# Performance work log

Hardware: AMD Instinct MI355X
Metric: run time of the kernel (lower is better)

## Reference

```python
import jax, jax.numpy as jnp
import numpy as np

DIM = 512
NUM_HEADS = 16
D_HEAD = DIM // NUM_HEADS
B, S = 4, 1024


def _relative_shift(pos_score):
    # pos_score: [B, H, S1, S2] -> Transformer-XL relative shift
    b, h, s1, s2 = pos_score.shape
    padded = jnp.pad(pos_score, ((0, 0), (0, 0), (0, 0), (1, 0)))  # [B,H,S1,S2+1]
    padded = padded.reshape(b, h, s2 + 1, s1)
    return padded[:, :, 1:].reshape(b, h, s1, s2)


def setup_inputs() -> dict:
    key = jax.random.key(0)
    ks = jax.random.split(key, 16)
    f32 = jnp.float32
    scale = 0.02
    inp = {
        "query": jax.random.normal(ks[0], (B, S, DIM), f32),
        "key": jax.random.normal(ks[1], (B, S, DIM), f32),
        "value": jax.random.normal(ks[2], (B, S, DIM), f32),
        "pos_embedding": jax.random.normal(ks[3], (B, S, DIM), f32),
        "Wq": jax.random.normal(ks[4], (DIM, DIM), f32) * scale,
        "bq": jnp.zeros((DIM,), f32),
        "Wk": jax.random.normal(ks[5], (DIM, DIM), f32) * scale,
        "bk": jnp.zeros((DIM,), f32),
        "Wv": jax.random.normal(ks[6], (DIM, DIM), f32) * scale,
        "bv": jnp.zeros((DIM,), f32),
        "Wp": jax.random.normal(ks[7], (DIM, DIM), f32) * scale,  # pos_proj, no bias
        "u_bias": jax.random.normal(ks[8], (NUM_HEADS, D_HEAD), f32) * scale,
        "v_bias": jax.random.normal(ks[9], (NUM_HEADS, D_HEAD), f32) * scale,
        "Wo": jax.random.normal(ks[10], (DIM, DIM), f32) * scale,
        "bo": jnp.zeros((DIM,), f32),
    }
    return inp


def reference(query, key, value, pos_embedding, Wq, bq, Wk, bk, Wv, bv, Wp,
              u_bias, v_bias, Wo, bo):
    b = query.shape[0]
    # projections (torch Linear: x @ W.T + b), split heads -> [B, S, H, Dh]
    q = (query @ Wq.T + bq).reshape(b, -1, NUM_HEADS, D_HEAD)
    k = (key @ Wk.T + bk).reshape(b, -1, NUM_HEADS, D_HEAD)
    v = (value @ Wv.T + bv).reshape(b, -1, NUM_HEADS, D_HEAD)
    p = (pos_embedding @ Wp.T).reshape(b, -1, NUM_HEADS, D_HEAD)

    # content score: (q + u) @ k^T  -> [B, H, Sq, Sk]
    content_score = jnp.einsum('bqhd,bkhd->bhqk', q + u_bias, k)
    # position score: (q + v) @ pos^T, then relative shift
    pos_score = jnp.einsum('bqhd,bkhd->bhqk', q + v_bias, p)
    pos_score = _relative_shift(pos_score)

    score = (content_score + pos_score) / np.sqrt(D_HEAD).astype(np.float32)
    attn = jax.nn.softmax(score, axis=-1)  # dropout_p = 0.0 -> identity

    context = jnp.einsum('bhqk,bkhd->bqhd', attn, v).reshape(b, -1, DIM)
    return context @ Wo.T + bo
```

## Files before the change

kernel.cpp:

```cpp
#include <hip/hip_runtime.h>
#include <hip/hip_bf16.h>
#include <math.h>


typedef float f32x4 __attribute__((ext_vector_type(4)));
typedef __bf16 bf16x8 __attribute__((ext_vector_type(8)));
typedef __bf16 bf16x2 __attribute__((ext_vector_type(2)));

#define MFMA16(a, b, c) __builtin_amdgcn_mfma_f32_16x16x32_bf16((a), (b), (c), 0, 0, 0)

constexpr int Bb  = 4;
constexpr int S   = 1024;
constexpr int H   = 16;
constexpr int Dh  = 32;
constexpr int DIM = 512;
constexpr float SCALEL2E = 0.25501818637084186f;
constexpr int ZROWS = 3 * S + 16;
constexpr size_t ZN = (size_t)64 * ZROWS * Dh;

constexpr size_t XN = (size_t)Bb * S * DIM;
constexpr size_t WN = (size_t)DIM * DIM;

__device__ inline bf16x8 cvt8(const float* __restrict__ p) {
  f32x4 a = *(const f32x4*)p;
  f32x4 b = *(const f32x4*)(p + 4);
  bf16x8 r;
  r[0] = (__bf16)a[0]; r[1] = (__bf16)a[1]; r[2] = (__bf16)a[2]; r[3] = (__bf16)a[3];
  r[4] = (__bf16)b[0]; r[5] = (__bf16)b[1]; r[6] = (__bf16)b[2]; r[7] = (__bf16)b[3];
  return r;
}

__device__ inline float fexp2(float x) {
  float r;
  asm("v_exp_f32 %0, %1" : "=v"(r) : "v"(x));
  return r;
}

__device__ inline void gload_lds16(const __bf16* g, __bf16* l) {
  __builtin_amdgcn_global_load_lds(
      (const __attribute__((address_space(1))) unsigned int*)g,
      (__attribute__((address_space(3))) unsigned int*)l, 16, 0, 0);
}

__global__ __launch_bounds__(256) void conv_kernel(
    const float* __restrict__ q, const float* __restrict__ k,
    const float* __restrict__ v, const float* __restrict__ p,
    const float* __restrict__ wq, const float* __restrict__ wk,
    const float* __restrict__ wv, const float* __restrict__ wp,
    const float* __restrict__ wo,
    __bf16* __restrict__ xb, __bf16* __restrict__ wb,
    __bf16* __restrict__ phZ)
{
  const int y = blockIdx.y;
  if (y >= 9) {
    const size_t i = (((size_t)(y - 9) * 1024 + blockIdx.x) * 256 + threadIdx.x) * 8;
    if (i < ZN) {
      bf16x8 zz = {};
      *(bf16x8*)(phZ + i) = zz;
    }
    return;
  }
  const float* src;
  size_t n;
  __bf16* dst;
  if (y < 4) {
    src = (y == 0) ? q : (y == 1) ? k : (y == 2) ? v : p;
    n = XN;
    dst = xb + (size_t)y * XN;
  } else {
    const int w = y - 4;
    src = (w == 0) ? wq : (w == 1) ? wk : (w == 2) ? wv : (w == 3) ? wp : wo;
    n = WN;
    dst = wb + (size_t)w * WN;
  }
  const size_t i = ((size_t)blockIdx.x * 256 + threadIdx.x) * 8;
  if (i >= n) return;
  *(bf16x8*)(dst + i) = cvt8(src + i);
}

__global__ __launch_bounds__(256) void gemm_kernel(
    const __bf16* __restrict__ xb, const __bf16* __restrict__ wb,
    const __bf16* __restrict__ ctxp,
    const float* __restrict__ bq, const float* __restrict__ bk,
    const float* __restrict__ bv, const float* __restrict__ bo,
    const float* __restrict__ ub, const float* __restrict__ vb,
    __bf16* __restrict__ qu, __bf16* __restrict__ qv,
    __bf16* __restrict__ kk, __bf16* __restrict__ vt,
    __bf16* __restrict__ phZ,
    float* __restrict__ outp, int mode)
{
  __shared__ __align__(16) __bf16 As[128 * 64];
  __shared__ __align__(16) __bf16 Bs[128 * 64];

  const int bid = blockIdx.x;
  const int u = bid >> 3;
  const int by = u & 3;
  const int idx = (bid & 7) + 8 * (u >> 2);
  int bx, z;
  if (mode == 0) { bx = idx & 31; z = idx >> 5; }
  else           { bx = idx;      z = 4; }

  const __bf16* Ag = (z < 4) ? (xb + (size_t)z * XN) : ctxp;
  const __bf16* Bg = wb + (size_t)z * WN;

  const int tid = threadIdx.x;
  const int wid = tid >> 6;
  const int ln = tid & 63;
  const int lm = ln & 15, lg = ln >> 4;
  const int wr = wid >> 1, wc = wid & 1;
  const int brow = bx * 128;
  const int bcol = by * 128;

  const int srow = ln >> 3;
  const int sc   = ln & 7;

  f32x4 acc[4][4] = {};

  for (int kt = 0; kt < DIM / 64; ++kt) {
    const int k0 = kt * 64;
#pragma unroll
    for (int i = 0; i < 4; ++i) {
      const int rb = wid * 32 + i * 8;
      const int r = rb + srow;
      const int cg = sc ^ (r & 7);
      gload_lds16(Ag + (size_t)(brow + r) * DIM + k0 + cg * 8, &As[rb * 64]);
      gload_lds16(Bg + (size_t)(bcol + r) * DIM + k0 + cg * 8, &Bs[rb * 64]);
    }
    __syncthreads();

#pragma unroll
    for (int ks = 0; ks < 2; ++ks) {
      bf16x8 a[4], b[4];
#pragma unroll
      for (int m = 0; m < 4; ++m) {
        const int row = wr * 64 + m * 16 + lm;
        const int cc = (ks * 4 + lg) ^ (row & 7);
        a[m] = *(const bf16x8*)&As[row * 64 + cc * 8];
      }
#pragma unroll
      for (int n = 0; n < 4; ++n) {
        const int row = wc * 64 + n * 16 + lm;
        const int cc = (ks * 4 + lg) ^ (row & 7);
        b[n] = *(const bf16x8*)&Bs[row * 64 + cc * 8];
      }
#pragma unroll
      for (int m = 0; m < 4; ++m)
#pragma unroll
        for (int n = 0; n < 4; ++n)
          acc[m][n] = MFMA16(a[m], b[n], acc[m][n]);
    }
    __syncthreads();
  }

#pragma unroll
  for (int n = 0; n < 4; ++n) {
    const int o = bcol + wc * 64 + n * 16 + lm;
    float bias = 0.f, ubv = 0.f, vbv = 0.f;
    if (z == 0) { bias = bq[o]; ubv = ub[o]; vbv = vb[o]; }
    else if (z == 1) bias = bk[o];
    else if (z == 2) bias = bv[o];
    else if (z == 4) bias = bo[o];
    const int h = o >> 5, d = o & 31;
#pragma unroll
    for (int m = 0; m < 4; ++m) {
#pragma unroll
      for (int r = 0; r < 4; ++r) {
        const int M = brow + wr * 64 + m * 16 + lg * 4 + r;
        const float val = acc[m][n][r];
        if (z == 4) {
          outp[(size_t)M * DIM + o] = val + bias;
          continue;
        }
        const int b = M >> 10, s = M & (S - 1);
        const int bh = b * H + h;
        if (z == 0) {
          const size_t idx2 = ((size_t)bh * S + s) * Dh + d;
          qu[idx2] = (__bf16)((val + bias + ubv) * SCALEL2E);
          qv[idx2] = (__bf16)((val + bias + vbv) * SCALEL2E);
        } else if (z == 1) {
          kk[((size_t)bh * S + s) * Dh + d] = (__bf16)(val + bias);
        } else if (z == 2) {
          const int t = s & 31;
          const int sp = (s & ~31) | ((t < 16) ? (t << 1) : ((t << 1) - 31));
          vt[((size_t)bh * Dh + d) * S + sp] = (__bf16)(val + bias);
        } else {
          phZ[((size_t)bh * ZROWS + (S + 1 + s)) * Dh + d] = (__bf16)val;
        }
      }
    }
  }
}

__global__ __launch_bounds__(256, 4) void attn_kernel(
    const __bf16* __restrict__ qu, const __bf16* __restrict__ qv,
    const __bf16* __restrict__ kk, const __bf16* __restrict__ vt,
    const __bf16* __restrict__ phZ,
    __bf16* __restrict__ ctx)
{
  __shared__ __align__(16) __bf16 kv_lds[4][2][1024];
  __shared__ __align__(16) __bf16 at_all[4][2][16 * 40];

  const int tid = threadIdx.x;
  const int wid = tid >> 6;
  const int l = tid & 63;
  const int lm = l & 15, lg = l >> 4;

  const int bid = blockIdx.x;
  const int bh = (bid & 7) + 8 * ((bid >> 3) & 7);
  const int q0 = (bid >> 6) * 64 + wid * 16;
  const int h = bh & (H - 1), b = bh >> 4;

  const __bf16* qub = qu + (size_t)bh * S * Dh;
  const __bf16* qvb = qv + (size_t)bh * S * Dh;
  const __bf16* kb  = kk + (size_t)bh * S * Dh;
  const __bf16* vtb = vt + (size_t)bh * Dh * S;
  const __bf16* pZb = phZ + (size_t)bh * ZROWS * Dh;
  const __bf16* pAb = pZb + (size_t)(S + 1) * Dh;

  const bf16x8 au  = *(const bf16x8*)(qub + (size_t)(q0 + lm) * Dh + lg * 8);
  const bf16x8 avA = *(const bf16x8*)(qvb + (size_t)(q0 + lm) * Dh + lg * 8);
  const bf16x8 avB = *(const bf16x8*)(qvb + (size_t)(q0 + 1 + lm) * Dh + lg * 8);

  int  slr[4];
  bool prd[4];
#pragma unroll
  for (int r = 0; r < 4; ++r) {
    const int qr = lg * 4 + r;
    slr[r] = (l & 48) | ((lm - qr + 15) & 15);
    prd[r] = (lm <= qr);
  }

  bf16x8 ones8;
#pragma unroll
  for (int i = 0; i < 8; ++i) ones8[i] = (__bf16)1.0f;

  f32x4 cta = {0.f,0.f,0.f,0.f}, ctb = {0.f,0.f,0.f,0.f};
  f32x4 ls  = {0.f,0.f,0.f,0.f};
  const f32x4 zero4 = {0.f,0.f,0.f,0.f};

  const int srow = l >> 2;
  const int scg  = ((l & 3) ^ (srow & 3)) * 8;
  auto stage = [&](int kt, int buf) {
    const __bf16* src;
    if (wid == 0)      src = kb  + (size_t)(kt + srow) * Dh + scg;
    else if (wid == 1) src = kb  + (size_t)(kt + 16 + srow) * Dh + scg;
    else if (wid == 2) src = vtb + (size_t)srow * S + kt + scg;
    else               src = vtb + (size_t)(16 + srow) * S + kt + scg;
    gload_lds16(src, &kv_lds[buf][wid >> 1][(wid & 1) * 512]);
  };

  const int cc = (lg ^ (lm & 3)) * 8;

  auto zwin = [&](int kt, bf16x8& z0, bf16x8& z1, bf16x8& z2, bool& uB) {
    const int ktc = (kt < S) ? kt : (S - 32);
    uB = (ktc > q0 - 31);
    const int mb = ktc - q0 + (S - 16);
    const __bf16* zb = uB ? pZb : pAb;
    z0 = *(const bf16x8*)(zb + (size_t)(mb + lm) * Dh + lg * 8);
    z1 = *(const bf16x8*)(zb + (size_t)(mb + 16 + lm) * Dh + lg * 8);
    z2 = *(const bf16x8*)(zb + (size_t)(mb + 32 + lm) * Dh + lg * 8);
  };

  auto half = [&](int kt, int tb, __bf16* at,
                  bf16x8 z0, bf16x8 z1, bf16x8 z2, bool uB) {
    const __bf16* Ks = kv_lds[tb][0];
    const __bf16* Vs = kv_lds[tb][1];
    bf16x8 kf0 = *(const bf16x8*)(Ks + lm * 32 + cc);
    bf16x8 kf1 = *(const bf16x8*)(Ks + (lm + 16) * 32 + cc);
    __builtin_amdgcn_s_setprio(1);
    f32x4 c0 = MFMA16(au, kf0, zero4);
    f32x4 c1 = MFMA16(au, kf1, zero4);
    const bf16x8 av = uB ? avB : avA;
    f32x4 pt0 = MFMA16(av, z0, zero4);
    f32x4 pt1 = MFMA16(av, z1, zero4);
    f32x4 pt2 = MFMA16(av, z2, zero4);
    __builtin_amdgcn_s_setprio(0);
    if (uB && (kt < q0 + 16)) {
      const int mb = kt - q0 + (S - 16);
      bf16x8 y0 = *(const bf16x8*)(pAb + (size_t)(mb + lm) * Dh + lg * 8);
      bf16x8 y1 = *(const bf16x8*)(pAb + (size_t)(mb + 16 + lm) * Dh + lg * 8);
      bf16x8 y2 = *(const bf16x8*)(pAb + (size_t)(mb + 32 + lm) * Dh + lg * 8);
      pt0 = MFMA16(avA, y0, pt0);
      pt1 = MFMA16(avA, y1, pt1);
      pt2 = MFMA16(avA, y2, pt2);
    }

#pragma unroll
    for (int r = 0; r < 4; ++r) {
      const float v0 = __shfl(pt0[r], slr[r], 64);
      const float v1 = __shfl(pt1[r], slr[r], 64);
      const float v2 = __shfl(pt2[r], slr[r], 64);
      const float s0 = c0[r] + (prd[r] ? v0 : v1);
      const float s1 = c1[r] + (prd[r] ? v1 : v2);
      bf16x2 pp;
      pp[0] = (__bf16)fexp2(s0);
      pp[1] = (__bf16)fexp2(s1);
      *(bf16x2*)(at + (lg * 4 + r) * 40 + 2 * lm) = pp;
    }

    bf16x8 af  = *(const bf16x8*)(at + lm * 40 + lg * 8);
    bf16x8 vf0 = *(const bf16x8*)(Vs + lm * 32 + cc);
    bf16x8 vf1 = *(const bf16x8*)(Vs + (lm + 16) * 32 + cc);
    __builtin_amdgcn_s_setprio(1);
    cta = MFMA16(af, vf0, cta);
    ctb = MFMA16(af, vf1, ctb);
    ls  = MFMA16(af, ones8, ls);
    __builtin_amdgcn_s_setprio(0);
  };

  __bf16* at0 = at_all[wid][0];
  __bf16* at1 = at_all[wid][1];

  bf16x8 zA0, zA1, zA2, zB0, zB1, zB2;
  bool uA, uB;
  zwin(0, zA0, zA1, zA2, uA);
  stage(0, 0);
  stage(32, 1);
  asm volatile("s_waitcnt vmcnt(0)" ::: "memory");
  __builtin_amdgcn_s_barrier();

  for (int kt = 0; kt < S; kt += 64) {
    const int t = kt >> 5;
    stage((kt + 64 < S) ? kt + 64 : kt, (t + 2) & 3);
    stage((kt + 96 < S) ? kt + 96 : kt, (t + 3) & 3);
    zwin(kt + 32, zB0, zB1, zB2, uB);
    half(kt, t & 3, at0, zA0, zA1, zA2, uA);
    zwin(kt + 64, zA0, zA1, zA2, uA);
    half(kt + 32, (t + 1) & 3, at1, zB0, zB1, zB2, uB);

    asm volatile("s_waitcnt vmcnt(3)" ::: "memory");
    __builtin_amdgcn_s_barrier();
  }

#pragma unroll
  for (int r = 0; r < 4; ++r) {
    const int s0 = q0 + lg * 4 + r;
    const float inv = 1.f / ls[r];
    __bf16* cp = ctx + ((size_t)b * S + s0) * DIM + h * Dh;
    cp[lm]      = (__bf16)(cta[r] * inv);
    cp[16 + lm] = (__bf16)(ctb[r] * inv);
  }
}

extern "C" void kernel_launch(void* const* d_in, const int* in_sizes, int n_in,
                              void* d_out, int out_size, void* d_ws, size_t ws_size,
                              hipStream_t stream) {
  const float* query = (const float*)d_in[0];
  const float* key   = (const float*)d_in[1];
  const float* value = (const float*)d_in[2];
  const float* pos   = (const float*)d_in[3];
  const float* Wq = (const float*)d_in[4];
  const float* bq = (const float*)d_in[5];
  const float* Wk = (const float*)d_in[6];
  const float* bk = (const float*)d_in[7];
  const float* Wv = (const float*)d_in[8];
  const float* bv = (const float*)d_in[9];
  const float* Wp = (const float*)d_in[10];
  const float* ub = (const float*)d_in[11];
  const float* vb = (const float*)d_in[12];
  const float* Wo = (const float*)d_in[13];
  const float* bo = (const float*)d_in[14];
  float* out = (float*)d_out;

  char* ws = (char*)d_ws;
  const size_t MB = 1ull << 20;
  __bf16* xb  = (__bf16*)(ws + 0 * MB);
  __bf16* wb  = (__bf16*)(ws + 16 * MB);
  __bf16* qu  = (__bf16*)(ws + 19 * MB);
  __bf16* qv  = (__bf16*)(ws + 23 * MB);
  __bf16* kk  = (__bf16*)(ws + 27 * MB);
  __bf16* vt  = (__bf16*)(ws + 31 * MB);
  __bf16* phZ = (__bf16*)(ws + 35 * MB);
  __bf16* ctx = (__bf16*)(ws + 48 * MB);

  conv_kernel<<<dim3(1024, 13), dim3(256), 0, stream>>>(
      query, key, value, pos, Wq, Wk, Wv, Wp, Wo, xb, wb, phZ);

  gemm_kernel<<<dim3(512), dim3(256), 0, stream>>>(
      xb, wb, ctx, bq, bk, bv, bo, ub, vb,
      qu, qv, kk, vt, phZ, out, 0);

  attn_kernel<<<dim3(1024), dim3(256), 0, stream>>>(
      qu, qv, kk, vt, phZ, ctx);

  gemm_kernel<<<dim3(128), dim3(256), 0, stream>>>(
      xb, wb, ctx, bq, bk, bv, bo, ub, vb,
      qu, qv, kk, vt, phZ, out, 1);
}
```

Measured before the change: 95.62 us.

## Trim phZ zeroing, coalesce V-transpose store, halve output GEMM tile, unpermute V

The zero-fill of the padded position buffer now writes only the boundary row windows the attention kernel reads, not the whole buffer. The V projection epilogue stages results through swizzled LDS so it can write the transposed V with 16-byte coalesced stores, and it drops the interleaved sequence permutation. The attention kernel now writes P in natural column order to match. The output GEMM is templated with a 64-row M tile and launches twice as many blocks to fill more CUs. The risk is that rows left uninitialized in phZ might be read, and that the layout change must agree exactly between the producer and consumer kernels.

```diff
diff --git a/kernel.cpp b/kernel.cpp
--- a/kernel.cpp
+++ b/kernel.cpp
@@ -5,7 +5,7 @@
 
 typedef float f32x4 __attribute__((ext_vector_type(4)));
 typedef __bf16 bf16x8 __attribute__((ext_vector_type(8)));
-typedef __bf16 bf16x2 __attribute__((ext_vector_type(2)));
+typedef __bf16 bf16x4 __attribute__((ext_vector_type(4)));
 
 #define MFMA16(a, b, c) __builtin_amdgcn_mfma_f32_16x16x32_bf16((a), (b), (c), 0, 0, 0)
 
@@ -16,7 +16,6 @@
 constexpr int DIM = 512;
 constexpr float SCALEL2E = 0.25501818637084186f;
 constexpr int ZROWS = 3 * S + 16;
-constexpr size_t ZN = (size_t)64 * ZROWS * Dh;
 
 constexpr size_t XN = (size_t)Bb * S * DIM;
 constexpr size_t WN = (size_t)DIM * DIM;
@@ -52,11 +51,15 @@
     __bf16* __restrict__ phZ)
 {
   const int y = blockIdx.y;
-  if (y >= 9) {
-    const size_t i = (((size_t)(y - 9) * 1024 + blockIdx.x) * 256 + threadIdx.x) * 8;
-    if (i < ZN) {
+  if (y == 9) {
+    const int e8 = blockIdx.x * 256 + threadIdx.x;
+    if (e8 < 64 * 136 * 4) {
+      const int rowIdx = e8 >> 2, chunk = e8 & 3;
+      const int bh = rowIdx / 136;
+      const int rl = rowIdx - bh * 136;
+      const int row = (rl < 72) ? (960 + rl) : (2040 + (rl - 72));
       bf16x8 zz = {};
-      *(bf16x8*)(phZ + i) = zz;
+      *(bf16x8*)(phZ + ((size_t)bh * ZROWS + row) * Dh + chunk * 8) = zz;
     }
     return;
   }
@@ -78,6 +81,7 @@
   *(bf16x8*)(dst + i) = cvt8(src + i);
 }
 
+template <int MODE>
 __global__ __launch_bounds__(256) void gemm_kernel(
     const __bf16* __restrict__ xb, const __bf16* __restrict__ wb,
     const __bf16* __restrict__ ctxp,
@@ -87,17 +91,21 @@
     __bf16* __restrict__ qu, __bf16* __restrict__ qv,
     __bf16* __restrict__ kk, __bf16* __restrict__ vt,
     __bf16* __restrict__ phZ,
-    float* __restrict__ outp, int mode)
+    float* __restrict__ outp)
 {
-  __shared__ __align__(16) __bf16 As[128 * 64];
-  __shared__ __align__(16) __bf16 Bs[128 * 64];
+  constexpr int MR = (MODE == 0) ? 4 : 2;
+  constexpr int BM = MR * 32;
+  __shared__ __align__(16) __bf16 smem[BM * 64 + 128 * 64];
+  __bf16* As = smem;
+  __bf16* Bs = smem + BM * 64;
+  __bf16* trans = smem;
 
   const int bid = blockIdx.x;
   const int u = bid >> 3;
   const int by = u & 3;
   const int idx = (bid & 7) + 8 * (u >> 2);
   int bx, z;
-  if (mode == 0) { bx = idx & 31; z = idx >> 5; }
+  if (MODE == 0) { bx = idx & 31; z = idx >> 5; }
   else           { bx = idx;      z = 4; }
 
   const __bf16* Ag = (z < 4) ? (xb + (size_t)z * XN) : ctxp;
@@ -108,32 +116,38 @@
   const int ln = tid & 63;
   const int lm = ln & 15, lg = ln >> 4;
   const int wr = wid >> 1, wc = wid & 1;
-  const int brow = bx * 128;
+  const int brow = bx * BM;
   const int bcol = by * 128;
 
   const int srow = ln >> 3;
   const int sc   = ln & 7;
 
-  f32x4 acc[4][4] = {};
+  f32x4 acc[MR][4] = {};
 
   for (int kt = 0; kt < DIM / 64; ++kt) {
     const int k0 = kt * 64;
+#pragma unroll
+    for (int i = 0; i < MR; ++i) {
+      const int rb = wid * (MR * 8) + i * 8;
+      const int r = rb + srow;
+      const int cg = sc ^ (r & 7);
+      gload_lds16(Ag + (size_t)(brow + r) * DIM + k0 + cg * 8, &As[rb * 64]);
+    }
 #pragma unroll
     for (int i = 0; i < 4; ++i) {
       const int rb = wid * 32 + i * 8;
       const int r = rb + srow;
       const int cg = sc ^ (r & 7);
-      gload_lds16(Ag + (size_t)(brow + r) * DIM + k0 + cg * 8, &As[rb * 64]);
       gload_lds16(Bg + (size_t)(bcol + r) * DIM + k0 + cg * 8, &Bs[rb * 64]);
     }
     __syncthreads();
 
 #pragma unroll
     for (int ks = 0; ks < 2; ++ks) {
-      bf16x8 a[4], b[4];
-#pragma unroll
-      for (int m = 0; m < 4; ++m) {
-        const int row = wr * 64 + m * 16 + lm;
+      bf16x8 a[MR], b[4];
+#pragma unroll
+      for (int m = 0; m < MR; ++m) {
+        const int row = wr * (MR * 16) + m * 16 + lm;
         const int cc = (ks * 4 + lg) ^ (row & 7);
         a[m] = *(const bf16x8*)&As[row * 64 + cc * 8];
       }
@@ -144,12 +158,45 @@
         b[n] = *(const bf16x8*)&Bs[row * 64 + cc * 8];
       }
 #pragma unroll
-      for (int m = 0; m < 4; ++m)
+      for (int m = 0; m < MR; ++m)
 #pragma unroll
         for (int n = 0; n < 4; ++n)
           acc[m][n] = MFMA16(a[m], b[n], acc[m][n]);
     }
     __syncthreads();
+  }
+
+  if (MODE == 0 && z == 2) {
+    const int b = brow >> 10;
+    const int sbase = brow & (S - 1);
+#pragma unroll
+    for (int n = 0; n < 4; ++n) {
+      const int dl = wc * 64 + n * 16 + lm;
+      const float bias = bv[bcol + dl];
+#pragma unroll
+      for (int m = 0; m < 4; ++m) {
+        const int sl = wr * 64 + m * 16 + lg * 4;
+        bf16x4 pk;
+#pragma unroll
+        for (int r = 0; r < 4; ++r) pk[r] = (__bf16)(acc[m][n][r] + bias);
+        const int base = dl * 128 + (((sl >> 3) ^ (dl & 15)) * 8) + (sl & 7);
+        *(bf16x4*)(trans + base) = pk;
+      }
+    }
+    __syncthreads();
+#pragma unroll
+    for (int j = 0; j < 4; ++j) {
+      const int dl = (tid >> 3) + j * 32;
+      const int d = dl & 31, hl = dl >> 5;
+      const int cp = (tid & 7) * 2;
+      bf16x8 v0 = *(const bf16x8*)(trans + dl * 128 + ((cp ^ (dl & 15)) * 8));
+      bf16x8 v1 = *(const bf16x8*)(trans + dl * 128 + (((cp + 1) ^ (dl & 15)) * 8));
+      const int bh2 = b * H + (bcol >> 5) + hl;
+      __bf16* dst = vt + ((size_t)bh2 * Dh + d) * S + sbase + cp * 8;
+      *(bf16x8*)dst = v0;
+      *(bf16x8*)(dst + 8) = v1;
+    }
+    return;
   }
 
 #pragma unroll
@@ -158,14 +205,13 @@
     float bias = 0.f, ubv = 0.f, vbv = 0.f;
     if (z == 0) { bias = bq[o]; ubv = ub[o]; vbv = vb[o]; }
     else if (z == 1) bias = bk[o];
-    else if (z == 2) bias = bv[o];
     else if (z == 4) bias = bo[o];
     const int h = o >> 5, d = o & 31;
 #pragma unroll
-    for (int m = 0; m < 4; ++m) {
+    for (int m = 0; m < MR; ++m) {
 #pragma unroll
       for (int r = 0; r < 4; ++r) {
-        const int M = brow + wr * 64 + m * 16 + lg * 4 + r;
+        const int M = brow + wr * (MR * 16) + m * 16 + lg * 4 + r;
         const float val = acc[m][n][r];
         if (z == 4) {
           outp[(size_t)M * DIM + o] = val + bias;
@@ -179,10 +225,6 @@
           qv[idx2] = (__bf16)((val + bias + vbv) * SCALEL2E);
         } else if (z == 1) {
           kk[((size_t)bh * S + s) * Dh + d] = (__bf16)(val + bias);
-        } else if (z == 2) {
-          const int t = s & 31;
-          const int sp = (s & ~31) | ((t < 16) ? (t << 1) : ((t << 1) - 31));
-          vt[((size_t)bh * Dh + d) * S + sp] = (__bf16)(val + bias);
         } else {
           phZ[((size_t)bh * ZROWS + (S + 1 + s)) * Dh + d] = (__bf16)val;
         }
@@ -292,10 +334,8 @@
       const float v2 = __shfl(pt2[r], slr[r], 64);
       const float s0 = c0[r] + (prd[r] ? v0 : v1);
       const float s1 = c1[r] + (prd[r] ? v1 : v2);
-      bf16x2 pp;
-      pp[0] = (__bf16)fexp2(s0);
-      pp[1] = (__bf16)fexp2(s1);
-      *(bf16x2*)(at + (lg * 4 + r) * 40 + 2 * lm) = pp;
+      at[(lg * 4 + r) * 40 + lm]      = (__bf16)fexp2(s0);
+      at[(lg * 4 + r) * 40 + 16 + lm] = (__bf16)fexp2(s1);
     }
 
     bf16x8 af  = *(const bf16x8*)(at + lm * 40 + lg * 8);
@@ -373,17 +413,17 @@
   __bf16* phZ = (__bf16*)(ws + 35 * MB);
   __bf16* ctx = (__bf16*)(ws + 48 * MB);
 
-  conv_kernel<<<dim3(1024, 13), dim3(256), 0, stream>>>(
+  conv_kernel<<<dim3(1024, 10), dim3(256), 0, stream>>>(
       query, key, value, pos, Wq, Wk, Wv, Wp, Wo, xb, wb, phZ);
 
-  gemm_kernel<<<dim3(512), dim3(256), 0, stream>>>(
+  gemm_kernel<0><<<dim3(512), dim3(256), 0, stream>>>(
       xb, wb, ctx, bq, bk, bv, bo, ub, vb,
-      qu, qv, kk, vt, phZ, out, 0);
+      qu, qv, kk, vt, phZ, out);
 
   attn_kernel<<<dim3(1024), dim3(256), 0, stream>>>(
       qu, qv, kk, vt, phZ, ctx);
 
-  gemm_kernel<<<dim3(128), dim3(256), 0, stream>>>(
+  gemm_kernel<1><<<dim3(256), dim3(256), 0, stream>>>(
       xb, wb, ctx, bq, bk, bv, bo, ub, vb,
-      qu, qv, kk, vt, phZ, out, 1);
-}
+      qu, qv, kk, vt, phZ, out);
+}
```

Result: faster. 89.28 us (-6.6%).
